# Kernel optimization log

Measured on AMD Instinct MI355X. Metric: run time of the kernel, lower is better.

Reference implementation:

```python
import jax, jax.numpy as jnp
import numpy as np

HEADS = 16


def setup_inputs() -> dict:
    key = jax.random.key(0)
    k1, k2, k3, k4 = jax.random.split(key, 4)
    B, S, D = 2, 2048, 1024
    x = jax.random.normal(k1, (B, S, D), dtype=jnp.float32)
    scale = 0.02
    Wq = jax.random.normal(k2, (D, D), dtype=jnp.float32) * scale
    Wk = jax.random.normal(k3, (D, D), dtype=jnp.float32) * scale
    Wv = jax.random.normal(k4, (D, D), dtype=jnp.float32) * scale
    return {"x": x, "Wq": Wq, "Wk": Wk, "Wv": Wv}


def reference(x, Wq, Wk, Wv):
    B, S, D = x.shape
    H = HEADS
    dh = D // H
    # project and split heads: (B, S, D) -> (B, H, S, dh)
    def split_heads(t):
        return t.reshape(B, S, H, dh).transpose(0, 2, 1, 3)

    q = split_heads(x @ Wq)
    k = split_heads(x @ Wk)
    v = split_heads(x @ Wv)

    # scores: (B, H, S, S)
    scores = jnp.einsum("bhqd,bhkd->bhqk", q, k)
    causal_mask = jnp.triu(jnp.ones((S, S), dtype=bool), k=1)  # True above diagonal -> masked
    scores = jnp.where(causal_mask, -jnp.inf, scores) / jnp.sqrt(jnp.float32(dh))
    weights = jax.nn.softmax(scores, axis=-1)
    # dropout is identity at inference (eval mode)
    ctx = jnp.einsum("bhqk,bhkd->bhqd", weights, v)  # (B, H, S, dh)
    return ctx.transpose(0, 2, 1, 3).reshape(B, S, D)
```

## Files before the change

### kernel.cpp

```cpp
#include <hip/hip_runtime.h>
#include <hip/hip_bf16.h>
#include <cstdint>

#define BATCH  2
#define SEQ    2048
#define DMODEL 1024
#define NH     16
#define DH     64

typedef short bf16x8 __attribute__((ext_vector_type(8)));
typedef float f32x4  __attribute__((ext_vector_type(4)));
typedef unsigned short u16;

#define MFMA16(a, b, c) __builtin_amdgcn_mfma_f32_16x16x32_bf16((a), (b), (c), 0, 0, 0)

#define GLL(gp, lp) __builtin_amdgcn_global_load_lds( \
    (const __attribute__((address_space(1))) void*)(gp), \
    (__attribute__((address_space(3))) void*)(lp), 16, 0, 0)

#define SCL 0.18033688011112042f

#if __has_builtin(__builtin_amdgcn_exp2f)
#define EXP2(x) __builtin_amdgcn_exp2f(x)
#else
#define EXP2(x) __expf((x) * 0.69314718055994531f)
#endif

static __device__ __forceinline__ u16 f2bf(float f) {
  union { float f; unsigned int i; } u; u.f = f;
  unsigned int r = u.i + 0x7FFFu + ((u.i >> 16) & 1u);
  return (u16)(r >> 16);
}

__global__ __launch_bounds__(256) void prep_kernel(const float* __restrict__ X,
                                                   const float* __restrict__ W0,
                                                   const float* __restrict__ W1,
                                                   const float* __restrict__ W2,
                                                   u16* __restrict__ Xb,
                                                   u16* __restrict__ Wt) {
  const int wg = blockIdx.x;
  const int t = threadIdx.x;
  if (wg < 2048) {
    int idx = (wg * 256 + t) * 8;
    float4 a = *reinterpret_cast<const float4*>(X + idx);
    float4 b = *reinterpret_cast<const float4*>(X + idx + 4);
    union { bf16x8 v; u16 u[8]; } pk;
    pk.u[0]=f2bf(a.x); pk.u[1]=f2bf(a.y); pk.u[2]=f2bf(a.z); pk.u[3]=f2bf(a.w);
    pk.u[4]=f2bf(b.x); pk.u[5]=f2bf(b.y); pk.u[6]=f2bf(b.z); pk.u[7]=f2bf(b.w);
    *reinterpret_cast<bf16x8*>(Xb + idx) = pk.v;
    return;
  }
  __shared__ float T[32][33];
  const int i = wg - 2048;
  const int z = i >> 10;
  const int rem = i & 1023;
  const int k0 = (rem & 31) * 32, n0 = (rem >> 5) * 32;
  const float* W = (z == 0) ? W0 : (z == 1) ? W1 : W2;
  const float sc = (z == 0) ? SCL : 1.0f;
  u16* out = Wt + (size_t)z * DMODEL * DMODEL;
  {
    int r = t >> 3, c = (t & 7) * 4;
    float4 v = *reinterpret_cast<const float4*>(W + (size_t)(k0 + r) * DMODEL + n0 + c);
    T[r][c] = v.x; T[r][c+1] = v.y; T[r][c+2] = v.z; T[r][c+3] = v.w;
  }
  __syncthreads();
  {
    int n = t >> 3, k = (t & 7) * 4;
    union { unsigned long long ll; u16 u[4]; } pk;
    pk.u[0] = f2bf(T[k][n] * sc);   pk.u[1] = f2bf(T[k+1][n] * sc);
    pk.u[2] = f2bf(T[k+2][n] * sc); pk.u[3] = f2bf(T[k+3][n] * sc);
    *reinterpret_cast<unsigned long long*>(out + (size_t)(n0 + n) * DMODEL + k0 + k) = pk.ll;
  }
}

__global__ __launch_bounds__(256) void qkv_mfma_kernel(const u16* __restrict__ Xb,
                                                       const u16* __restrict__ Wt,
                                                       u16* __restrict__ Y) {
  __shared__ u16 As[128 * 64];
  __shared__ u16 Bs[128 * 64];
  char* Ab = (char*)As; char* Bb = (char*)Bs;
  const int t = threadIdx.x;
  const int lane = t & 63;
  const int w = t >> 6;
  const int wr = w >> 1, wc = w & 1;
  const int l15 = lane & 15, lg = lane >> 4;
  const int row0 = blockIdx.x * 128;
  const int col0 = blockIdx.y * 128;
  const int z = blockIdx.z;
  const u16* Wz = Wt + (size_t)z * DMODEL * DMODEL;
  u16* Yz = Y + (size_t)z * ((size_t)BATCH * SEQ * DMODEL);

  f32x4 acc[4][4];
  #pragma unroll
  for (int mt = 0; mt < 4; ++mt)
    #pragma unroll
    for (int nt = 0; nt < 4; ++nt)
      acc[mt][nt] = (f32x4){0.f, 0.f, 0.f, 0.f};

  size_t aofs[4], bofs[4];
  #pragma unroll
  for (int it = 0; it < 4; ++it) {
    int row = it * 32 + (t >> 3);
    int sl  = (t & 7) ^ (row & 7);
    aofs[it] = (size_t)(row0 + row) * DMODEL + sl * 8;
    bofs[it] = (size_t)(col0 + row) * DMODEL + sl * 8;
  }

  for (int k0 = 0; k0 < DMODEL; k0 += 64) {
    __syncthreads();
    #pragma unroll
    for (int it = 0; it < 4; ++it) {
      GLL(Xb + aofs[it] + k0, Ab + it * 4096 + w * 1024);
      GLL(Wz + bofs[it] + k0, Bb + it * 4096 + w * 1024);
    }
    __syncthreads();
    #pragma unroll
    for (int c = 0; c < 2; ++c) {
      bf16x8 am[4], bn[4];
      int kof = c * 64 + lg * 16;
      #pragma unroll
      for (int mt = 0; mt < 4; ++mt) {
        int row = wr * 64 + mt * 16 + l15;
        am[mt] = *reinterpret_cast<const bf16x8*>(Ab + row * 128 + (kof ^ ((row & 7) << 4)));
      }
      #pragma unroll
      for (int nt = 0; nt < 4; ++nt) {
        int row = wc * 64 + nt * 16 + l15;
        bn[nt] = *reinterpret_cast<const bf16x8*>(Bb + row * 128 + (kof ^ ((row & 7) << 4)));
      }
      #pragma unroll
      for (int mt = 0; mt < 4; ++mt)
        #pragma unroll
        for (int nt = 0; nt < 4; ++nt)
          acc[mt][nt] = MFMA16(am[mt], bn[nt], acc[mt][nt]);
    }
  }

  #pragma unroll
  for (int mt = 0; mt < 4; ++mt) {
    #pragma unroll
    for (int i = 0; i < 4; ++i) {
      int bs = row0 + wr * 64 + mt * 16 + lg * 4 + i;
      int b = bs >> 11, s = bs & (SEQ - 1);
      #pragma unroll
      for (int nt = 0; nt < 4; ++nt) {
        int d = col0 + wc * 64 + nt * 16 + l15;
        int h = d >> 6, dd = d & (DH - 1);
        size_t off = (((size_t)b * NH + h) * SEQ + s) * DH + dd;
        Yz[off] = f2bf(acc[mt][nt][i]);
      }
    }
  }
}

__global__ __launch_bounds__(256) void transpose_v_kernel(const u16* __restrict__ V,
                                                          u16* __restrict__ Vt) {
  __shared__ u16 L[64][72];
  const int sb = blockIdx.x, h = blockIdx.y, b = blockIdx.z;
  const size_t hin  = ((size_t)b * NH + h) * (size_t)SEQ * DH;
  const size_t hout = ((size_t)b * NH + h) * (size_t)DH * SEQ;
  const int s0 = sb * 64;
  const int t = threadIdx.x;
  const int r = t >> 3, c = t & 7;
  #pragma unroll
  for (int it = 0; it < 2; ++it) {
    int row = r + it * 32;
    bf16x8 v = *reinterpret_cast<const bf16x8*>(V + hin + (size_t)(s0 + row) * DH + c * 8);
    *reinterpret_cast<bf16x8*>(&L[row][c * 8]) = v;
  }
  __syncthreads();
  #pragma unroll
  for (int it = 0; it < 2; ++it) {
    int d = r + it * 32;
    union { bf16x8 v; u16 u[8]; } pk;
    #pragma unroll
    for (int j = 0; j < 8; ++j) pk.u[j] = L[c * 8 + j][d];
    *reinterpret_cast<bf16x8*>(Vt + hout + (size_t)d * SEQ + s0 + c * 8) = pk.v;
  }
}

#define STAGE_KV(kb)                                                  \
  {                                                                   \
    const u16* kp_ = Kw + hq + (size_t)(kb) * (64 * DH);              \
    const u16* vp_ = Vt + hv + (size_t)(kb) * 64;                     \
    char* kd_ = (char*)Ks + dstb;                                     \
    char* vd_ = (char*)Vs + dstb;                                     \
    GLL(kp_ + kofs0, kd_);        GLL(vp_ + vofs0, vd_);              \
    GLL(kp_ + kofs1, kd_ + 1024); GLL(vp_ + vofs1, vd_ + 1024);       \
  }

__global__ __launch_bounds__(256) void flash_mfma14_kernel(const u16* __restrict__ Qw,
                                                           const u16* __restrict__ Kw,
                                                           const u16* __restrict__ Vt,
                                                           float* __restrict__ Out) {
  __shared__ u16 Ks[64 * 64];
  __shared__ u16 Vs[64 * 64];
  __shared__ u16 Pl[4][16 * 64];
  const int wgid = blockIdx.x;
  const int g = wgid & 31;
  const int j = (wgid >> 5) & 7;
  const int r = wgid >> 8;
  const int qt = r * 8 + ((r & 1) ? (7 - j) : j);
  const int b = g >> 4, h = g & 15;
  const int nkv = qt + 1;

  const int t = threadIdx.x, lane = t & 63, w = t >> 6;
  const int l15 = lane & 15, lg = lane >> 4;
  char* Pb = (char*)Pl[w];
  const size_t hq = ((size_t)b * NH + h) * (size_t)SEQ * DH;
  const size_t hv = ((size_t)b * NH + h) * (size_t)DH * SEQ;

  int kofs0, kofs1, vofs0, vofs1;
  {
    int i0 = (w * 2 + 0) * 64 + lane, i1 = (w * 2 + 1) * 64 + lane;
    int r0 = i0 >> 3, s0 = i0 & 7;
    int r1 = i1 >> 3, s1 = i1 & 7;
    kofs0 = r0 * DH  + ((s0 ^ (r0 & 7)) * 8);
    kofs1 = r1 * DH  + ((s1 ^ (r1 & 7)) * 8);
    vofs0 = r0 * SEQ + ((s0 ^ (r0 & 7)) * 8);
    vofs1 = r1 * SEQ + ((s1 ^ (r1 & 7)) * 8);
  }
  const int dstb = w * 2048;

  const int csel = (l15 & 4) << 4;
  const int sw45 = (lg * 16) ^ ((l15 & 3) << 4);
  const int rb0  = l15 * 128 + sw45 + csel;
  const int rb1  = rb0 ^ 64;
  const int pw0  = l15 * 128 + ((lg * 8) ^ ((l15 & 1) << 4));
  const int xw   = ((l15 >> 1) & 3) << 5;

  const int q0 = qt * 64;
  const int qrow = q0 + w * 16 + l15;

  bf16x8 qf0, qf1;
  {
    const u16* qp = Qw + hq + (size_t)qrow * DH + lg * 8;
    qf0 = *reinterpret_cast<const bf16x8*>(qp);
    qf1 = *reinterpret_cast<const bf16x8*>(qp + 32);
  }

  f32x4 o[4];
  #pragma unroll
  for (int dt = 0; dt < 4; ++dt) o[dt] = (f32x4){0.f, 0.f, 0.f, 0.f};
  float l_ = 0.f;

  #pragma unroll 1
  for (int kb = 0; kb < nkv - 1; ++kb) {
    __syncthreads();
    STAGE_KV(kb);
    __syncthreads();

    float s[4][4];
    __builtin_amdgcn_s_setprio(1);
    #pragma unroll
    for (int kt = 0; kt < 4; ++kt) {
      f32x4 sa = (f32x4){0.f, 0.f, 0.f, 0.f};
      bf16x8 kf0 = *reinterpret_cast<const bf16x8*>((char*)Ks + rb0 + kt * 2048);
      bf16x8 kf1 = *reinterpret_cast<const bf16x8*>((char*)Ks + rb1 + kt * 2048);
      sa = MFMA16(kf0, qf0, sa);
      sa = MFMA16(kf1, qf1, sa);
      #pragma unroll
      for (int i = 0; i < 4; ++i) s[kt][i] = sa[i];
    }
    __builtin_amdgcn_s_setprio(0);

    #pragma unroll
    for (int kt = 0; kt < 4; ++kt) {
      union { unsigned long long ll; __hip_bfloat16 bf[4]; } pk;
      #pragma unroll
      for (int i = 0; i < 4; ++i) {
        float e = EXP2(s[kt][i]);
        l_ += e;
        pk.bf[i] = __float2bfloat16(e);
      }
      *reinterpret_cast<unsigned long long*>(Pb + pw0 + ((kt * 32) ^ xw)) = pk.ll;
    }

    __builtin_amdgcn_s_setprio(1);
    {
      bf16x8 pa0 = *reinterpret_cast<const bf16x8*>(Pb + rb0);
      bf16x8 pa1 = *reinterpret_cast<const bf16x8*>(Pb + rb1);
      #pragma unroll
      for (int dt = 0; dt < 4; ++dt) {
        bf16x8 v0 = *reinterpret_cast<const bf16x8*>((char*)Vs + rb0 + dt * 2048);
        bf16x8 v1 = *reinterpret_cast<const bf16x8*>((char*)Vs + rb1 + dt * 2048);
        o[dt] = MFMA16(pa0, v0, o[dt]);
        o[dt] = MFMA16(pa1, v1, o[dt]);
      }
    }
    __builtin_amdgcn_s_setprio(0);
  }

  {
    const int kb = nkv - 1;
    const int k0 = kb * 64;
    __syncthreads();
    STAGE_KV(kb);
    __syncthreads();

    const int ktlim = w + 1;
    const int kcmax = (w + 2) >> 1;

    float s[4][4];
    #pragma unroll
    for (int kt = 0; kt < 4; ++kt) {
      if (kt < ktlim) {
        f32x4 sa = (f32x4){0.f, 0.f, 0.f, 0.f};
        bf16x8 kf0 = *reinterpret_cast<const bf16x8*>((char*)Ks + rb0 + kt * 2048);
        bf16x8 kf1 = *reinterpret_cast<const bf16x8*>((char*)Ks + rb1 + kt * 2048);
        sa = MFMA16(kf0, qf0, sa);
        sa = MFMA16(kf1, qf1, sa);
        #pragma unroll
        for (int i = 0; i < 4; ++i) {
          int key = k0 + kt * 16 + lg * 4 + i;
          s[kt][i] = (key > qrow) ? -1e30f : sa[i];
        }
      } else {
        s[kt][0] = -1e30f; s[kt][1] = -1e30f; s[kt][2] = -1e30f; s[kt][3] = -1e30f;
      }
    }

    #pragma unroll
    for (int kt = 0; kt < 4; ++kt) {
      union { unsigned long long ll; __hip_bfloat16 bf[4]; } pk;
      #pragma unroll
      for (int i = 0; i < 4; ++i) {
        float e = EXP2(s[kt][i]);
        l_ += e;
        pk.bf[i] = __float2bfloat16(e);
      }
      *reinterpret_cast<unsigned long long*>(Pb + pw0 + ((kt * 32) ^ xw)) = pk.ll;
    }

    bf16x8 pa0 = *reinterpret_cast<const bf16x8*>(Pb + rb0);
    bf16x8 pa1 = *reinterpret_cast<const bf16x8*>(Pb + rb1);
    #pragma unroll
    for (int kc = 0; kc < 2; ++kc) {
      if (kc >= kcmax) break;
      const int off = kc ? (rb1 - rb0) : 0;
      #pragma unroll
      for (int dt = 0; dt < 4; ++dt) {
        bf16x8 vv = *reinterpret_cast<const bf16x8*>((char*)Vs + rb0 + off + dt * 2048);
        o[dt] = MFMA16(kc ? pa1 : pa0, vv, o[dt]);
      }
    }
  }

  l_ += __shfl_xor(l_, 16);
  l_ += __shfl_xor(l_, 32);
  #pragma unroll
  for (int i = 0; i < 4; ++i) {
    float li = __shfl(l_, (lane & 48) + lg * 4 + i);
    float inv = 1.f / li;
    int q = q0 + w * 16 + lg * 4 + i;
    float* op = Out + ((size_t)b * SEQ + q) * DMODEL + h * DH + l15;
    #pragma unroll
    for (int dt = 0; dt < 4; ++dt) op[dt * 16] = o[dt][i] * inv;
  }
}

extern "C" void kernel_launch(void* const* d_in, const int* in_sizes, int n_in,
                              void* d_out, int out_size, void* d_ws, size_t ws_size,
                              hipStream_t stream) {
  const float* x  = (const float*)d_in[0];
  const float* Wq = (const float*)d_in[1];
  const float* Wk = (const float*)d_in[2];
  const float* Wv = (const float*)d_in[3];
  float* out = (float*)d_out;

  u16* ws  = (u16*)d_ws;
  u16* qkv = ws;
  u16* xb  = ws + 12582912;
  u16* wt  = ws + 16777216;
  u16* vt  = ws + 19922944;

  prep_kernel<<<5120, 256, 0, stream>>>(x, Wq, Wk, Wv, xb, wt);
  qkv_mfma_kernel<<<dim3(32, 8, 3), 256, 0, stream>>>(xb, wt, qkv);
  transpose_v_kernel<<<dim3(32, NH, BATCH), 256, 0, stream>>>(qkv + 8388608, vt);
  flash_mfma14_kernel<<<1024, 256, 0, stream>>>(qkv, qkv + 4194304, vt, out);
}
```

Baseline: 81.85 us.

## Double-buffer K/V tiles in flash kernel with async prefetch of next block

Doubles the shared-memory K and V buffers and issues the global-to-LDS load for the next key block before computing on the current one. Explicit vmcnt waits and raw s_barriers replace the two __syncthreads per iteration, so load latency can overlap the QK, softmax and PV work. The cost is twice the LDS for K/V, which may lower occupancy, plus reliance on hand-tuned waitcnt values being correct.

```diff
diff --git a/kernel.cpp b/kernel.cpp
--- a/kernel.cpp
+++ b/kernel.cpp
@@ -179,22 +179,91 @@
   }
 }
 
-#define STAGE_KV(kb)                                                  \
+#define BAR()                                  \
+  __builtin_amdgcn_sched_barrier(0);           \
+  __builtin_amdgcn_s_barrier();                \
+  __builtin_amdgcn_sched_barrier(0)
+
+#define WAITC(N)                                                      \
+  asm volatile("s_waitcnt vmcnt(" #N ")" ::: "memory");               \
+  __builtin_amdgcn_sched_barrier(0)
+
+#define STAGE_KV(buf, kb)                                             \
   {                                                                   \
     const u16* kp_ = Kw + hq + (size_t)(kb) * (64 * DH);              \
     const u16* vp_ = Vt + hv + (size_t)(kb) * 64;                     \
-    char* kd_ = (char*)Ks + dstb;                                     \
-    char* vd_ = (char*)Vs + dstb;                                     \
+    char* kd_ = (char*)(Ks[buf]) + dstb;                              \
+    char* vd_ = (char*)(Vs[buf]) + dstb;                              \
     GLL(kp_ + kofs0, kd_);        GLL(vp_ + vofs0, vd_);              \
     GLL(kp_ + kofs1, kd_ + 1024); GLL(vp_ + vofs1, vd_ + 1024);       \
   }
 
-__global__ __launch_bounds__(256) void flash_mfma14_kernel(const u16* __restrict__ Qw,
+#define TILE(kbv, KB, VB, MASKED)                                                    \
+  {                                                                                  \
+    char* Kb = (char*)(KB);                                                          \
+    char* Vb = (char*)(VB);                                                          \
+    const int k0_ = (kbv) * 64;                                                      \
+    const int ktlim_ = (MASKED) ? (w + 1) : 4;                                       \
+    const int kcmax_ = (MASKED) ? ((w + 2) >> 1) : 2;                                \
+    float s[4][4];                                                                   \
+    __builtin_amdgcn_s_setprio(1);                                                   \
+    _Pragma("unroll")                                                                \
+    for (int kt = 0; kt < 4; ++kt) {                                                 \
+      if (kt < ktlim_) {                                                             \
+        f32x4 sa = (f32x4){0.f, 0.f, 0.f, 0.f};                                      \
+        bf16x8 kf0 = *reinterpret_cast<const bf16x8*>(Kb + rb0 + kt * 2048);         \
+        bf16x8 kf1 = *reinterpret_cast<const bf16x8*>(Kb + rb1 + kt * 2048);         \
+        sa = MFMA16(kf0, qf0, sa);                                                   \
+        sa = MFMA16(kf1, qf1, sa);                                                   \
+        _Pragma("unroll")                                                            \
+        for (int i = 0; i < 4; ++i) {                                                \
+          float sv = sa[i];                                                          \
+          if (MASKED) {                                                              \
+            int key = k0_ + kt * 16 + lg * 4 + i;                                    \
+            if (key > qrow) sv = -1e30f;                                             \
+          }                                                                          \
+          s[kt][i] = sv;                                                             \
+        }                                                                            \
+      } else {                                                                       \
+        s[kt][0] = -1e30f; s[kt][1] = -1e30f; s[kt][2] = -1e30f; s[kt][3] = -1e30f;  \
+      }                                                                              \
+    }                                                                                \
+    __builtin_amdgcn_s_setprio(0);                                                   \
+    _Pragma("unroll")                                                                \
+    for (int kt = 0; kt < 4; ++kt) {                                                 \
+      union { unsigned long long ll; __hip_bfloat16 bf[4]; } pk;                     \
+      _Pragma("unroll")                                                              \
+      for (int i = 0; i < 4; ++i) {                                                  \
+        float e = EXP2(s[kt][i]);                                                    \
+        l_ += e;                                                                     \
+        pk.bf[i] = __float2bfloat16(e);                                              \
+      }                                                                              \
+      *reinterpret_cast<unsigned long long*>(Pb + pw0 + ((kt * 32) ^ xw)) = pk.ll;   \
+    }                                                                                \
+    __builtin_amdgcn_s_setprio(1);                                                   \
+    {                                                                                \
+      bf16x8 pa0 = *reinterpret_cast<const bf16x8*>(Pb + rb0);                       \
+      bf16x8 pa1 = *reinterpret_cast<const bf16x8*>(Pb + rb1);                       \
+      _Pragma("unroll")                                                              \
+      for (int kc = 0; kc < 2; ++kc) {                                               \
+        if (kc >= kcmax_) break;                                                     \
+        const int off_ = kc ? (rb1 - rb0) : 0;                                       \
+        _Pragma("unroll")                                                            \
+        for (int dt = 0; dt < 4; ++dt) {                                             \
+          bf16x8 vv = *reinterpret_cast<const bf16x8*>(Vb + rb0 + off_ + dt * 2048); \
+          o[dt] = MFMA16(kc ? pa1 : pa0, vv, o[dt]);                                 \
+        }                                                                            \
+      }                                                                              \
+    }                                                                                \
+    __builtin_amdgcn_s_setprio(0);                                                   \
+  }
+
+__global__ __launch_bounds__(256) void flash_mfma15_kernel(const u16* __restrict__ Qw,
                                                            const u16* __restrict__ Kw,
                                                            const u16* __restrict__ Vt,
                                                            float* __restrict__ Out) {
-  __shared__ u16 Ks[64 * 64];
-  __shared__ u16 Vs[64 * 64];
+  __shared__ u16 Ks[2][64 * 64];
+  __shared__ u16 Vs[2][64 * 64];
   __shared__ u16 Pl[4][16 * 64];
   const int wgid = blockIdx.x;
   const int g = wgid & 31;
@@ -244,106 +313,22 @@
   for (int dt = 0; dt < 4; ++dt) o[dt] = (f32x4){0.f, 0.f, 0.f, 0.f};
   float l_ = 0.f;
 
+  STAGE_KV(0, 0);
+  int kb = 0;
   #pragma unroll 1
-  for (int kb = 0; kb < nkv - 1; ++kb) {
-    __syncthreads();
-    STAGE_KV(kb);
-    __syncthreads();
-
-    float s[4][4];
-    __builtin_amdgcn_s_setprio(1);
-    #pragma unroll
-    for (int kt = 0; kt < 4; ++kt) {
-      f32x4 sa = (f32x4){0.f, 0.f, 0.f, 0.f};
-      bf16x8 kf0 = *reinterpret_cast<const bf16x8*>((char*)Ks + rb0 + kt * 2048);
-      bf16x8 kf1 = *reinterpret_cast<const bf16x8*>((char*)Ks + rb1 + kt * 2048);
-      sa = MFMA16(kf0, qf0, sa);
-      sa = MFMA16(kf1, qf1, sa);
-      #pragma unroll
-      for (int i = 0; i < 4; ++i) s[kt][i] = sa[i];
-    }
-    __builtin_amdgcn_s_setprio(0);
-
-    #pragma unroll
-    for (int kt = 0; kt < 4; ++kt) {
-      union { unsigned long long ll; __hip_bfloat16 bf[4]; } pk;
-      #pragma unroll
-      for (int i = 0; i < 4; ++i) {
-        float e = EXP2(s[kt][i]);
-        l_ += e;
-        pk.bf[i] = __float2bfloat16(e);
-      }
-      *reinterpret_cast<unsigned long long*>(Pb + pw0 + ((kt * 32) ^ xw)) = pk.ll;
-    }
-
-    __builtin_amdgcn_s_setprio(1);
-    {
-      bf16x8 pa0 = *reinterpret_cast<const bf16x8*>(Pb + rb0);
-      bf16x8 pa1 = *reinterpret_cast<const bf16x8*>(Pb + rb1);
-      #pragma unroll
-      for (int dt = 0; dt < 4; ++dt) {
-        bf16x8 v0 = *reinterpret_cast<const bf16x8*>((char*)Vs + rb0 + dt * 2048);
-        bf16x8 v1 = *reinterpret_cast<const bf16x8*>((char*)Vs + rb1 + dt * 2048);
-        o[dt] = MFMA16(pa0, v0, o[dt]);
-        o[dt] = MFMA16(pa1, v1, o[dt]);
-      }
-    }
-    __builtin_amdgcn_s_setprio(0);
-  }
-
-  {
-    const int kb = nkv - 1;
-    const int k0 = kb * 64;
-    __syncthreads();
-    STAGE_KV(kb);
-    __syncthreads();
-
-    const int ktlim = w + 1;
-    const int kcmax = (w + 2) >> 1;
-
-    float s[4][4];
-    #pragma unroll
-    for (int kt = 0; kt < 4; ++kt) {
-      if (kt < ktlim) {
-        f32x4 sa = (f32x4){0.f, 0.f, 0.f, 0.f};
-        bf16x8 kf0 = *reinterpret_cast<const bf16x8*>((char*)Ks + rb0 + kt * 2048);
-        bf16x8 kf1 = *reinterpret_cast<const bf16x8*>((char*)Ks + rb1 + kt * 2048);
-        sa = MFMA16(kf0, qf0, sa);
-        sa = MFMA16(kf1, qf1, sa);
-        #pragma unroll
-        for (int i = 0; i < 4; ++i) {
-          int key = k0 + kt * 16 + lg * 4 + i;
-          s[kt][i] = (key > qrow) ? -1e30f : sa[i];
-        }
-      } else {
-        s[kt][0] = -1e30f; s[kt][1] = -1e30f; s[kt][2] = -1e30f; s[kt][3] = -1e30f;
-      }
-    }
-
-    #pragma unroll
-    for (int kt = 0; kt < 4; ++kt) {
-      union { unsigned long long ll; __hip_bfloat16 bf[4]; } pk;
-      #pragma unroll
-      for (int i = 0; i < 4; ++i) {
-        float e = EXP2(s[kt][i]);
-        l_ += e;
-        pk.bf[i] = __float2bfloat16(e);
-      }
-      *reinterpret_cast<unsigned long long*>(Pb + pw0 + ((kt * 32) ^ xw)) = pk.ll;
-    }
-
-    bf16x8 pa0 = *reinterpret_cast<const bf16x8*>(Pb + rb0);
-    bf16x8 pa1 = *reinterpret_cast<const bf16x8*>(Pb + rb1);
-    #pragma unroll
-    for (int kc = 0; kc < 2; ++kc) {
-      if (kc >= kcmax) break;
-      const int off = kc ? (rb1 - rb0) : 0;
-      #pragma unroll
-      for (int dt = 0; dt < 4; ++dt) {
-        bf16x8 vv = *reinterpret_cast<const bf16x8*>((char*)Vs + rb0 + off + dt * 2048);
-        o[dt] = MFMA16(kc ? pa1 : pa0, vv, o[dt]);
-      }
-    }
+  for (; kb < nkv - 1; ++kb) {
+    const int cur = kb & 1;
+    STAGE_KV(cur ^ 1, kb + 1);
+    WAITC(4);
+    BAR();
+    TILE(kb, Ks[cur], Vs[cur], 0);
+    BAR();
+  }
+  {
+    const int cur = kb & 1;
+    WAITC(0);
+    BAR();
+    TILE(kb, Ks[cur], Vs[cur], 1);
   }
 
   l_ += __shfl_xor(l_, 16);
@@ -377,5 +362,5 @@
   prep_kernel<<<5120, 256, 0, stream>>>(x, Wq, Wk, Wv, xb, wt);
   qkv_mfma_kernel<<<dim3(32, 8, 3), 256, 0, stream>>>(xb, wt, qkv);
   transpose_v_kernel<<<dim3(32, NH, BATCH), 256, 0, stream>>>(qkv + 8388608, vt);
-  flash_mfma14_kernel<<<1024, 256, 0, stream>>>(qkv, qkv + 4194304, vt, out);
-}
+  flash_mfma15_kernel<<<1024, 256, 0, stream>>>(qkv, qkv + 4194304, vt, out);
+}
```

New measurement: 82.20 us. Within noise of the previous version (+0.4%).
